# Performance work log

Measured on AMD Instinct MI355X. Metric: run time of the kernel, lower is better.

Reference implementation:

```python
import jax, jax.numpy as jnp
import numpy as np

N, D, F, E, K = 8192, 1024, 4096, 8, 2


def setup_inputs() -> dict:
    key = jax.random.key(0)
    ks = jax.random.split(key, 4)
    x = jax.random.normal(ks[0], (N, D), dtype=jnp.float32)
    Wg = jax.random.normal(ks[1], (D, E), dtype=jnp.float32) * 0.02
    W1 = jax.random.normal(ks[2], (E, D, F), dtype=jnp.float32) * 0.02
    b1 = jnp.zeros((E, F), dtype=jnp.float32)
    W2 = jax.random.normal(ks[3], (E, F, D), dtype=jnp.float32) * 0.02
    b2 = jnp.zeros((E, D), dtype=jnp.float32)
    return {"x": x, "Wg": Wg, "W1": W1, "b1": b1, "W2": W2, "b2": b2}


def reference(x, Wg, W1, b1, W2, b2):
    # Top-k softmax gate (TopKGate): pick K experts per token, renormalize.
    logits = x @ Wg                                        # [N, E]
    probs = jax.nn.softmax(logits, axis=-1)
    gate_vals, expert_idx = jax.lax.top_k(probs, K)        # [N, K]
    gate_w = gate_vals / jnp.sum(gate_vals, axis=-1, keepdims=True)

    # Expert FFN (dispatch/combine math): the torch code sorts tokens by expert
    # id, all-to-alls them to the owning rank, applies the local Expert MLP,
    # and combines back weighted by gate_w. The jit-friendly equivalent is to
    # compute every expert's MLP for all tokens and gather the selected rows.
    h = jax.nn.relu(jnp.einsum('nd,edf->enf', x, W1) + b1[:, None, :])  # [E, N, F]
    o = jnp.einsum('enf,efd->end', h, W2) + b2[:, None, :]               # [E, N, D]

    tok = jnp.arange(x.shape[0])
    sel = o[expert_idx, tok[:, None]]                      # [N, K, D]
    y = jnp.sum(gate_w[..., None] * sel, axis=1)           # [N, D]
    return y
```

## Files before the change

kernel.cpp:

```cpp
#include <hip/hip_runtime.h>

#define N_TOK 8192
#define DIM   1024
#define FFN   4096
#define NEXP  8
#define TOPK  2
#define NENT  (N_TOK * TOPK)
#define MAXM  20

using short8  = __attribute__((ext_vector_type(8))) short;
using floatx4 = __attribute__((ext_vector_type(4))) float;

__device__ __forceinline__ unsigned short f2bf(float f) {
    union { float f; unsigned u; } v; v.f = f;
    unsigned r = v.u + 0x7fffu + ((v.u >> 16) & 1u);
    return (unsigned short)(r >> 16);
}

#define GLOAD_LDS16(gptr, lptr) __builtin_amdgcn_global_load_lds( \
    (__attribute__((address_space(1))) void*)(void*)(gptr),       \
    (__attribute__((address_space(3))) void*)(lptr), 16, 0, 0)


__global__ __launch_bounds__(256) void prep_kernel(
    const float* __restrict__ W1, const float* __restrict__ W2,
    unsigned short* __restrict__ w1t, unsigned short* __restrict__ w2t,
    const float* __restrict__ x, const float* __restrict__ wg,
    unsigned short* __restrict__ xb,
    int* __restrict__ topk_e, float* __restrict__ topk_w,
    int* __restrict__ counts)
{
    __shared__ float tile[64][65];
    int bid = blockIdx.x;
    int tid = threadIdx.x;

    if (bid < 16384) {
        const float* in; unsigned short* out; int R, C, e, c0, r0;
        if (bid < 8192) {
            in = W1; out = w1t; R = DIM; C = FFN;
            e = bid >> 10; int b = bid & 1023;
            c0 = (b & 63) * 64; r0 = (b >> 6) * 64;
        } else {
            int bb = bid - 8192;
            in = W2; out = w2t; R = FFN; C = DIM;
            e = bb >> 10; int b = bb & 1023;
            c0 = (b & 15) * 64; r0 = (b >> 4) * 64;
        }
        const float* inp = in + (size_t)e * DIM * FFN;
        unsigned short* outp = out + (size_t)e * DIM * FFN;
        int lrow = tid >> 4;
        int lc4  = (tid & 15) * 4;
#pragma unroll
        for (int i = 0; i < 4; i++) {
            int r = i * 16 + lrow;
            float4 v = *(const float4*)&inp[(size_t)(r0 + r) * C + c0 + lc4];
            tile[r][lc4 + 0] = v.x;
            tile[r][lc4 + 1] = v.y;
            tile[r][lc4 + 2] = v.z;
            tile[r][lc4 + 3] = v.w;
        }
        __syncthreads();
        int r4 = (tid & 15) * 4;
#pragma unroll
        for (int i = 0; i < 4; i++) {
            int c = i * 16 + (tid >> 4);
            ushort4 o;
            o.x = f2bf(tile[r4 + 0][c]);
            o.y = f2bf(tile[r4 + 1][c]);
            o.z = f2bf(tile[r4 + 2][c]);
            o.w = f2bf(tile[r4 + 3][c]);
            *(ushort4*)&outp[(size_t)(c0 + c) * R + r0 + r4] = o;
        }
        return;
    }

    int wave = tid >> 6, lane = tid & 63;
    int t = (bid - 16384) * 4 + wave;
    const float* xr = x + (size_t)t * DIM;
    unsigned short* xbr = xb + (size_t)t * DIM;
    float acc[NEXP];
#pragma unroll
    for (int e = 0; e < NEXP; e++) acc[e] = 0.f;
    for (int it = 0; it < DIM / 256; it++) {
        int d = it * 256 + lane * 4;
        float4 xv = *(const float4*)&xr[d];
        ushort4 ub;
        ub.x = f2bf(xv.x); ub.y = f2bf(xv.y); ub.z = f2bf(xv.z); ub.w = f2bf(xv.w);
        *(ushort4*)&xbr[d] = ub;
        const float* wp = wg + (size_t)d * NEXP;
#pragma unroll
        for (int j = 0; j < 4; j++) {
            float xj = (j == 0) ? xv.x : (j == 1) ? xv.y : (j == 2) ? xv.z : xv.w;
            const float4* wr = (const float4*)(wp + j * NEXP);
            float4 w0 = wr[0], w1 = wr[1];
            acc[0] += xj * w0.x; acc[1] += xj * w0.y; acc[2] += xj * w0.z; acc[3] += xj * w0.w;
            acc[4] += xj * w1.x; acc[5] += xj * w1.y; acc[6] += xj * w1.z; acc[7] += xj * w1.w;
        }
    }
#pragma unroll
    for (int e = 0; e < NEXP; e++) {
#pragma unroll
        for (int off = 32; off > 0; off >>= 1) acc[e] += __shfl_xor(acc[e], off);
    }
    if (lane == 0) {
        int e1 = 0; float l1 = acc[0];
        for (int e = 1; e < NEXP; e++) if (acc[e] > l1) { l1 = acc[e]; e1 = e; }
        int e2 = -1; float l2 = -3.4e38f;
        for (int e = 0; e < NEXP; e++) if (e != e1 && acc[e] > l2) { l2 = acc[e]; e2 = e; }
        float w1v = 1.f / (1.f + expf(l2 - l1));
        topk_e[t * 2]     = e1;  topk_e[t * 2 + 1] = e2;
        topk_w[t * 2]     = w1v; topk_w[t * 2 + 1] = 1.f - w1v;
        atomicAdd(&counts[e1], 1);
        atomicAdd(&counts[e2], 1);
    }
}

__global__ __launch_bounds__(256) void scatter_kernel(const int* __restrict__ topk_e,
                                                      const float* __restrict__ topk_w,
                                                      const int* __restrict__ counts,
                                                      int* __restrict__ offs,
                                                      int* __restrict__ cursors,
                                                      int* __restrict__ entry_token,
                                                      float* __restrict__ entry_w) {
    int off_[NEXP]; int s = 0;
#pragma unroll
    for (int e = 0; e < NEXP; e++) { off_[e] = s; s += counts[e]; }
    if (blockIdx.x == 0 && threadIdx.x == 0) {
#pragma unroll
        for (int e = 0; e < NEXP; e++) offs[e] = off_[e];
        offs[NEXP] = s;
    }
    int t = blockIdx.x * 256 + threadIdx.x;
#pragma unroll
    for (int k = 0; k < TOPK; k++) {
        int e = topk_e[t * 2 + k];
        int pos = off_[e] + atomicAdd(&cursors[e], 1);
        entry_token[pos] = t;
        entry_w[pos] = topk_w[t * 2 + k];
    }
}


__global__ __launch_bounds__(256, 3) void gemm1_kernel(
    const unsigned short* __restrict__ xb,
    const unsigned short* __restrict__ w1t,
    const float* __restrict__ b1,
    const int* __restrict__ offs,
    const int* __restrict__ entry_token,
    unsigned short* __restrict__ h)
{
    int bid   = blockIdx.x;
    int xcd   = bid & 7;
    int inner = bid >> 3;
    int gq    = inner / MAXM;
    int mt    = inner - gq * MAXM;
    int g     = gq * 8 + xcd;
    int e     = g >> 5;
    int nt    = g & 31;
    int base = offs[e];
    int cnt  = offs[e + 1] - base;
    int m0   = mt * 128;
    if (m0 >= cnt) return;
    int f0   = nt * 128;

    __shared__ unsigned short As[2][128 * 32];
    __shared__ unsigned short Bs[2][128 * 32];
    __shared__ int toks[128];

    int tid = threadIdx.x;
    if (tid < 128) {
        int r = m0 + tid;
        toks[tid] = entry_token[base + (r < cnt ? r : 0)];
    }
    __syncthreads();

    int wave = tid >> 6, lane = tid & 63;
    int wm = (wave >> 1) * 64, wn = (wave & 1) * 64;

    int lr = lane >> 2, sl = lane & 3;
    int g0 = (sl ^ ((lr >> 1) & 3)) * 8;
    const unsigned short* aG[2];
    const unsigned short* bG[2];
    int ldsOff[2];
#pragma unroll
    for (int c = 0; c < 2; c++) {
        int row = wave * 32 + c * 16 + lr;
        aG[c] = xb + (size_t)toks[row] * DIM + g0;
        bG[c] = w1t + ((size_t)e * FFN + f0 + row) * DIM + g0;
        ldsOff[c] = (wave * 32 + c * 16) * 32;
    }

    floatx4 acc[4][4];
#pragma unroll
    for (int i = 0; i < 4; i++)
#pragma unroll
        for (int j = 0; j < 4; j++) acc[i][j] = (floatx4)0.f;

    int quad = lane >> 4, rm = lane & 15;
    int slf  = (quad ^ ((rm >> 1) & 3)) * 8;
    int arow = (wm + rm) * 32;
    int brow = (wn + rm) * 32;

#pragma unroll
    for (int c = 0; c < 2; c++) {
        GLOAD_LDS16(aG[c], &As[0][ldsOff[c]]);
        GLOAD_LDS16(bG[c], &Bs[0][ldsOff[c]]);
        aG[c] += 32; bG[c] += 32;
    }

    int cur = 0;
    for (int kk = 0; kk < DIM / 32; kk++) {
        __syncthreads();
        short8 af[4], bfr[4];
#pragma unroll
        for (int mi = 0; mi < 4; mi++) af[mi] = *(const short8*)&As[cur][arow + mi * 512 + slf];
#pragma unroll
        for (int ni = 0; ni < 4; ni++) bfr[ni] = *(const short8*)&Bs[cur][brow + ni * 512 + slf];
        if (kk + 1 < DIM / 32) {
            int nxt = cur ^ 1;
#pragma unroll
            for (int c = 0; c < 2; c++) {
                GLOAD_LDS16(aG[c], &As[nxt][ldsOff[c]]);
                GLOAD_LDS16(bG[c], &Bs[nxt][ldsOff[c]]);
                aG[c] += 32; bG[c] += 32;
            }
        }
#pragma unroll
        for (int mi = 0; mi < 4; mi++)
#pragma unroll
            for (int ni = 0; ni < 4; ni++)
                acc[mi][ni] = __builtin_amdgcn_mfma_f32_16x16x32_bf16(af[mi], bfr[ni], acc[mi][ni], 0, 0, 0);
        cur ^= 1;
    }

#pragma unroll
    for (int mi = 0; mi < 4; mi++) {
        int mbase = wm + mi * 16 + quad * 4;
#pragma unroll
        for (int ni = 0; ni < 4; ni++) {
            int f = f0 + wn + ni * 16 + rm;
            float bias = b1[e * FFN + f];
            floatx4 v = acc[mi][ni];
#pragma unroll
            for (int r = 0; r < 4; r++) {
                int row = m0 + mbase + r;
                if (row < cnt) {
                    float t = v[r] + bias;
                    t = t > 0.f ? t : 0.f;
                    h[(size_t)(base + row) * FFN + f] = f2bf(t);
                }
            }
        }
    }
}


__global__ __launch_bounds__(256, 3) void gemm2_kernel(
    const unsigned short* __restrict__ h,
    const unsigned short* __restrict__ w2t,
    const float* __restrict__ b2,
    const int* __restrict__ offs,
    const int* __restrict__ entry_token,
    const float* __restrict__ entry_w,
    float* __restrict__ y)
{
    int bid  = blockIdx.x;
    int e    = bid & 7;
    int grp  = bid % (8 * MAXM);
    int mt   = grp >> 3;
    int nt   = bid / (8 * MAXM);
    int base = offs[e];
    int cnt  = offs[e + 1] - base;
    int m0   = mt * 128;
    if (m0 >= cnt) return;
    int n0   = nt * 128;

    __shared__ unsigned short As[2][128 * 32];
    __shared__ unsigned short Bs[2][128 * 32];

    int tid = threadIdx.x;
    int wave = tid >> 6, lane = tid & 63;
    int wm = (wave >> 1) * 64, wn = (wave & 1) * 64;

    int lr = lane >> 2, sl = lane & 3;
    int g0 = (sl ^ ((lr >> 1) & 3)) * 8;
    const unsigned short* aG[2];
    const unsigned short* bG[2];
    int ldsOff[2];
#pragma unroll
    for (int c = 0; c < 2; c++) {
        int row = wave * 32 + c * 16 + lr;
        aG[c] = h + (size_t)(base + m0 + row) * FFN + g0;
        bG[c] = w2t + ((size_t)e * DIM + n0 + row) * FFN + g0;
        ldsOff[c] = (wave * 32 + c * 16) * 32;
    }

    floatx4 acc[4][4];
#pragma unroll
    for (int i = 0; i < 4; i++)
#pragma unroll
        for (int j = 0; j < 4; j++) acc[i][j] = (floatx4)0.f;

    int quad = lane >> 4, rm = lane & 15;
    int slf  = (quad ^ ((rm >> 1) & 3)) * 8;
    int arow = (wm + rm) * 32;
    int brow = (wn + rm) * 32;

#pragma unroll
    for (int c = 0; c < 2; c++) {
        GLOAD_LDS16(aG[c], &As[0][ldsOff[c]]);
        GLOAD_LDS16(bG[c], &Bs[0][ldsOff[c]]);
        aG[c] += 32; bG[c] += 32;
    }

    int cur = 0;
    for (int kk = 0; kk < FFN / 32; kk++) {
        __syncthreads();
        short8 af[4], bfr[4];
#pragma unroll
        for (int mi = 0; mi < 4; mi++) af[mi] = *(const short8*)&As[cur][arow + mi * 512 + slf];
#pragma unroll
        for (int ni = 0; ni < 4; ni++) bfr[ni] = *(const short8*)&Bs[cur][brow + ni * 512 + slf];
        if (kk + 1 < FFN / 32) {
            int nxt = cur ^ 1;
#pragma unroll
            for (int c = 0; c < 2; c++) {
                GLOAD_LDS16(aG[c], &As[nxt][ldsOff[c]]);
                GLOAD_LDS16(bG[c], &Bs[nxt][ldsOff[c]]);
                aG[c] += 32; bG[c] += 32;
            }
        }
#pragma unroll
        for (int mi = 0; mi < 4; mi++)
#pragma unroll
            for (int ni = 0; ni < 4; ni++)
                acc[mi][ni] = __builtin_amdgcn_mfma_f32_16x16x32_bf16(af[mi], bfr[ni], acc[mi][ni], 0, 0, 0);
        cur ^= 1;
    }

    float bs[4];
#pragma unroll
    for (int ni = 0; ni < 4; ni++) bs[ni] = b2[e * DIM + n0 + wn + ni * 16 + rm];
#pragma unroll
    for (int mi = 0; mi < 4; mi++) {
        int mbase = wm + mi * 16 + quad * 4;
#pragma unroll
        for (int r = 0; r < 4; r++) {
            int row = m0 + mbase + r;
            if (row < cnt) {
                int tok = entry_token[base + row];
                float w = entry_w[base + row];
                float* yr = y + (size_t)tok * DIM;
#pragma unroll
                for (int ni = 0; ni < 4; ni++) {
                    int n = n0 + wn + ni * 16 + rm;
                    atomicAdd(&yr[n], w * (acc[mi][ni][r] + bs[ni]));
                }
            }
        }
    }
}


extern "C" void kernel_launch(void* const* d_in, const int* in_sizes, int n_in,
                              void* d_out, int out_size, void* d_ws, size_t ws_size,
                              hipStream_t stream) {
    const float* x  = (const float*)d_in[0];
    const float* Wg = (const float*)d_in[1];
    const float* W1 = (const float*)d_in[2];
    const float* b1 = (const float*)d_in[3];
    const float* W2 = (const float*)d_in[4];
    const float* b2 = (const float*)d_in[5];
    float* y = (float*)d_out;

    char* p = (char*)d_ws;
    unsigned short* xb  = (unsigned short*)p; p += (size_t)N_TOK * DIM * 2;
    unsigned short* w1t = (unsigned short*)p; p += (size_t)NEXP * DIM * FFN * 2;
    unsigned short* w2t = (unsigned short*)p; p += (size_t)NEXP * DIM * FFN * 2;
    unsigned short* h   = (unsigned short*)p; p += (size_t)(NENT + 128) * FFN * 2;
    int*   topk_e      = (int*)p;   p += (size_t)N_TOK * TOPK * 4;
    float* topk_w      = (float*)p; p += (size_t)N_TOK * TOPK * 4;
    int*   entry_token = (int*)p;   p += (size_t)NENT * 4;
    float* entry_w     = (float*)p; p += (size_t)NENT * 4;
    int*   counts      = (int*)p;   p += NEXP * 4;
    int*   cursors     = (int*)p;   p += NEXP * 4;
    int*   offs        = (int*)p;   p += (NEXP + 1) * 4;

    hipMemsetAsync(counts, 0, NEXP * 4 * 2, stream);
    hipMemsetAsync(y, 0, (size_t)N_TOK * DIM * 4, stream);

    prep_kernel<<<16384 + N_TOK / 4, 256, 0, stream>>>(W1, W2, w1t, w2t, x, Wg, xb,
                                                       topk_e, topk_w, counts);
    scatter_kernel<<<N_TOK / 256, 256, 0, stream>>>(topk_e, topk_w, counts, offs,
                                                    cursors, entry_token, entry_w);
    gemm1_kernel<<<NEXP * MAXM * (FFN / 128), 256, 0, stream>>>(xb, w1t, b1, offs, entry_token, h);
    gemm2_kernel<<<NEXP * MAXM * (DIM / 128), 256, 0, stream>>>(h, w2t, b2, offs,
                                                                entry_token, entry_w, y);
}
```

Measured before the change: 0.9995 ms.

## Move W2 transpose into gemm1 launch and widen transpose tiles

The W2 fp32-to-bf16 transpose moves out of the prep kernel and into extra leading blocks of the gemm1 launch, so it can overlap with the expert GEMM instead of running before it. Both transposes now use a 256x32 tile with an XOR-swizzled shared buffer, float4 stores into LDS and 16-byte bf16 output stores, replacing the padded 64x64 tile with 4-element writes. gemm1 shares its LDS between the GEMM buffers and the transpose tile through a union. In exchange the gemm1 grid grows and the transpose blocks compete with GEMM blocks for CUs.

```diff
diff --git a/kernel.cpp b/kernel.cpp
--- a/kernel.cpp
+++ b/kernel.cpp
@@ -8,8 +8,9 @@
 #define NENT  (N_TOK * TOPK)
 #define MAXM  20
 
-using short8  = __attribute__((ext_vector_type(8))) short;
-using floatx4 = __attribute__((ext_vector_type(4))) float;
+using short8   = __attribute__((ext_vector_type(8))) short;
+using ushort8v = __attribute__((ext_vector_type(8))) unsigned short;
+using floatx4  = __attribute__((ext_vector_type(4))) float;
 
 __device__ __forceinline__ unsigned short f2bf(float f) {
     union { float f; unsigned u; } v; v.f = f;
@@ -22,60 +23,58 @@
     (__attribute__((address_space(3))) void*)(lptr), 16, 0, 0)
 
 
+__device__ __forceinline__ void transpose_tile(const float* __restrict__ inp,
+                                               unsigned short* __restrict__ outp,
+                                               int R, int C, int r0, int c0,
+                                               float* __restrict__ tile) {
+    int t = threadIdx.x;
+    int p = t & 7;
+    int trow = t >> 3;
+    int w = t >> 6;
+#pragma unroll
+    for (int i = 0; i < 8; i++) {
+        int r = i * 32 + trow;
+        float4 v = *(const float4*)&inp[(size_t)(r0 + r) * C + c0 + p * 4];
+        int cc = p ^ ((4 * i + w) & 7);
+        *(float4*)&tile[r * 32 + cc * 4] = v;
+    }
+    __syncthreads();
+    int c = t >> 3;
+    int cbase = ((c >> 2) ^ p) * 4 + (c & 3);
+    unsigned short* orow = outp + (size_t)(c0 + c) * R + r0;
+#pragma unroll
+    for (int j = 0; j < 4; j++) {
+        int rb = j * 64 + p * 8;
+        ushort8v us;
+#pragma unroll
+        for (int k = 0; k < 8; k++)
+            us[k] = f2bf(tile[(rb + k) * 32 + cbase]);
+        *(ushort8v*)&orow[rb] = us;
+    }
+}
+
+
 __global__ __launch_bounds__(256) void prep_kernel(
-    const float* __restrict__ W1, const float* __restrict__ W2,
-    unsigned short* __restrict__ w1t, unsigned short* __restrict__ w2t,
+    const float* __restrict__ W1, unsigned short* __restrict__ w1t,
     const float* __restrict__ x, const float* __restrict__ wg,
     unsigned short* __restrict__ xb,
     int* __restrict__ topk_e, float* __restrict__ topk_w,
     int* __restrict__ counts)
 {
-    __shared__ float tile[64][65];
+    __shared__ float tile[8192];
     int bid = blockIdx.x;
+    if (bid < 4096) {
+        int rt = bid & 3;
+        int ct = (bid >> 2) & 127;
+        int e  = bid >> 9;
+        transpose_tile(W1 + (size_t)e * DIM * FFN, w1t + (size_t)e * DIM * FFN,
+                       DIM, FFN, rt * 256, ct * 32, tile);
+        return;
+    }
+
     int tid = threadIdx.x;
-
-    if (bid < 16384) {
-        const float* in; unsigned short* out; int R, C, e, c0, r0;
-        if (bid < 8192) {
-            in = W1; out = w1t; R = DIM; C = FFN;
-            e = bid >> 10; int b = bid & 1023;
-            c0 = (b & 63) * 64; r0 = (b >> 6) * 64;
-        } else {
-            int bb = bid - 8192;
-            in = W2; out = w2t; R = FFN; C = DIM;
-            e = bb >> 10; int b = bb & 1023;
-            c0 = (b & 15) * 64; r0 = (b >> 4) * 64;
-        }
-        const float* inp = in + (size_t)e * DIM * FFN;
-        unsigned short* outp = out + (size_t)e * DIM * FFN;
-        int lrow = tid >> 4;
-        int lc4  = (tid & 15) * 4;
-#pragma unroll
-        for (int i = 0; i < 4; i++) {
-            int r = i * 16 + lrow;
-            float4 v = *(const float4*)&inp[(size_t)(r0 + r) * C + c0 + lc4];
-            tile[r][lc4 + 0] = v.x;
-            tile[r][lc4 + 1] = v.y;
-            tile[r][lc4 + 2] = v.z;
-            tile[r][lc4 + 3] = v.w;
-        }
-        __syncthreads();
-        int r4 = (tid & 15) * 4;
-#pragma unroll
-        for (int i = 0; i < 4; i++) {
-            int c = i * 16 + (tid >> 4);
-            ushort4 o;
-            o.x = f2bf(tile[r4 + 0][c]);
-            o.y = f2bf(tile[r4 + 1][c]);
-            o.z = f2bf(tile[r4 + 2][c]);
-            o.w = f2bf(tile[r4 + 3][c]);
-            *(ushort4*)&outp[(size_t)(c0 + c) * R + r0 + r4] = o;
-        }
-        return;
-    }
-
     int wave = tid >> 6, lane = tid & 63;
-    int t = (bid - 16384) * 4 + wave;
+    int t = (bid - 4096) * 4 + wave;
     const float* xr = x + (size_t)t * DIM;
     unsigned short* xbr = xb + (size_t)t * DIM;
     float acc[NEXP];
@@ -115,6 +114,7 @@
     }
 }
 
+
 __global__ __launch_bounds__(256) void scatter_kernel(const int* __restrict__ topk_e,
                                                       const float* __restrict__ topk_w,
                                                       const int* __restrict__ counts,
@@ -141,15 +141,33 @@
 }
 
 
+union __align__(16) G1Smem {
+    struct { unsigned short As[2][4096]; unsigned short Bs[2][4096]; int toks[128]; } g;
+    float tile[8192];
+};
+
 __global__ __launch_bounds__(256, 3) void gemm1_kernel(
     const unsigned short* __restrict__ xb,
     const unsigned short* __restrict__ w1t,
     const float* __restrict__ b1,
     const int* __restrict__ offs,
     const int* __restrict__ entry_token,
-    unsigned short* __restrict__ h)
+    unsigned short* __restrict__ h,
+    const float* __restrict__ W2,
+    unsigned short* __restrict__ w2t)
 {
-    int bid   = blockIdx.x;
+    __shared__ G1Smem sm;
+    int bid0 = blockIdx.x;
+    if (bid0 < 4096) {
+        int rt = bid0 & 15;
+        int ct = (bid0 >> 4) & 31;
+        int e  = bid0 >> 9;
+        transpose_tile(W2 + (size_t)e * DIM * FFN, w2t + (size_t)e * DIM * FFN,
+                       FFN, DIM, rt * 256, ct * 32, sm.tile);
+        return;
+    }
+
+    int bid   = bid0 - 4096;
     int xcd   = bid & 7;
     int inner = bid >> 3;
     int gq    = inner / MAXM;
@@ -163,9 +181,9 @@
     if (m0 >= cnt) return;
     int f0   = nt * 128;
 
-    __shared__ unsigned short As[2][128 * 32];
-    __shared__ unsigned short Bs[2][128 * 32];
-    __shared__ int toks[128];
+    auto& As   = sm.g.As;
+    auto& Bs   = sm.g.Bs;
+    auto& toks = sm.g.toks;
 
     int tid = threadIdx.x;
     if (tid < 128) {
@@ -389,11 +407,12 @@
     hipMemsetAsync(counts, 0, NEXP * 4 * 2, stream);
     hipMemsetAsync(y, 0, (size_t)N_TOK * DIM * 4, stream);
 
-    prep_kernel<<<16384 + N_TOK / 4, 256, 0, stream>>>(W1, W2, w1t, w2t, x, Wg, xb,
-                                                       topk_e, topk_w, counts);
+    prep_kernel<<<4096 + N_TOK / 4, 256, 0, stream>>>(W1, w1t, x, Wg, xb,
+                                                      topk_e, topk_w, counts);
     scatter_kernel<<<N_TOK / 256, 256, 0, stream>>>(topk_e, topk_w, counts, offs,
                                                     cursors, entry_token, entry_w);
-    gemm1_kernel<<<NEXP * MAXM * (FFN / 128), 256, 0, stream>>>(xb, w1t, b1, offs, entry_token, h);
+    gemm1_kernel<<<4096 + NEXP * MAXM * (FFN / 128), 256, 0, stream>>>(
+        xb, w1t, b1, offs, entry_token, h, W2, w2t);
     gemm2_kernel<<<NEXP * MAXM * (DIM / 128), 256, 0, stream>>>(h, w2t, b2, offs,
                                                                 entry_token, entry_w, y);
 }
```

Result: no change. 992.5 us (-0.7%).
